# Optimization experiments

Measured on AMD Instinct MI355X. Metric: run time of the kernel, lower is better.

The kernel has to match this reference:

```python
import jax, jax.numpy as jnp
import numpy as np

WH, WW = 7, 7
N_TOK = WH * WW


def _buffers():
    # relative_coords_table: [1, 2*WH-1, 2*WW-1, 2], Swin-V2 log-spaced coords
    ch = np.arange(-(WH - 1), WH, dtype=np.float32)
    cw = np.arange(-(WW - 1), WW, dtype=np.float32)
    t = np.stack(np.meshgrid(ch, cw, indexing='ij'), axis=-1)[None]
    t[..., 0] /= (WH - 1)
    t[..., 1] /= (WW - 1)
    t *= 8.0
    t = np.sign(t) * np.log2(np.abs(t) + 1.0) / np.log2(8.0)
    # relative_position_index: [N, N]
    coords = np.stack(np.meshgrid(np.arange(WH), np.arange(WW), indexing='ij'))
    cf = coords.reshape(2, -1)
    rc = (cf[:, :, None] - cf[:, None, :]).transpose(1, 2, 0).astype(np.int32)
    rc[..., 0] += WH - 1
    rc[..., 1] += WW - 1
    rc[..., 0] *= 2 * WW - 1
    idx = rc.sum(-1)
    return jnp.asarray(t, jnp.float32), jnp.asarray(idx, jnp.int32)


def setup_inputs() -> dict:
    key = jax.random.key(0)
    ks = jax.random.split(key, 10)
    C, H = 384, 12
    B_, nW = 2048, 64
    rel_table, rel_index = _buffers()
    s = 0.02
    return {
        'x': jax.random.normal(ks[0], (B_, N_TOK, C), jnp.float32),
        'mask': jax.random.normal(ks[1], (nW, N_TOK, N_TOK), jnp.float32),
        'qkv_w': jax.random.normal(ks[2], (3 * C, C), jnp.float32) * s,
        'q_bias': jnp.zeros((C,), jnp.float32),
        'v_bias': jnp.zeros((C,), jnp.float32),
        'logit_scale': jnp.full((H, 1, 1), np.log(10.0), jnp.float32),
        'cpb_w1': jax.random.normal(ks[3], (512, 2), jnp.float32) * s,
        'cpb_b1': jnp.zeros((512,), jnp.float32),
        'cpb_w2': jax.random.normal(ks[4], (H, 512), jnp.float32) * s,
        'proj_w': jax.random.normal(ks[5], (C, C), jnp.float32) * s,
        'proj_b': jnp.zeros((C,), jnp.float32),
        'rel_table': rel_table,
        'rel_index': rel_index,
    }


def reference(x, mask, qkv_w, q_bias, v_bias, logit_scale, cpb_w1, cpb_b1,
              cpb_w2, proj_w, proj_b, rel_table, rel_index):
    B_, N, C = x.shape
    H = logit_scale.shape[0]
    Dh = C // H
    nW = mask.shape[0]
    # qkv projection with q/v bias, zero bias for k
    qkv_bias = jnp.concatenate([q_bias, jnp.zeros_like(v_bias), v_bias])
    qkv = x @ qkv_w.T + qkv_bias                       # [B, N, 3C]
    qkv = qkv.reshape(B_, N, 3, H, Dh).transpose(2, 0, 3, 1, 4)
    q, k, v = qkv[0], qkv[1], qkv[2]                    # [B, H, N, Dh]
    # per-head clamped logit scale
    ls = jnp.exp(jnp.minimum(logit_scale, np.log(1.0 / 0.01)))  # [H,1,1]
    # continuous relative position bias via small MLP
    tbl = jax.nn.relu(rel_table @ cpb_w1.T + cpb_b1) @ cpb_w2.T  # [1,13,13,H]
    tbl = tbl.reshape(-1, H)
    rpb = tbl[rel_index.reshape(-1)].reshape(N, N, H).transpose(2, 0, 1)
    rpb = 16.0 * jax.nn.sigmoid(rpb)                    # [H, N, N]
    # cosine attention (kernel uses norm + 1e-6 in denominator)
    qn = q / (jnp.sqrt(jnp.sum(q * q, -1, keepdims=True)) + 1e-6)
    kn = k / (jnp.sqrt(jnp.sum(k * k, -1, keepdims=True)) + 1e-6)
    attn = jnp.einsum('bhnd,bhmd->bhnm', qn, kn) * ls[None]
    attn = attn + rpb[None]
    # shift mask: window index w = batch_index % nW
    attn = attn.reshape(B_ // nW, nW, H, N, N) + mask[None, :, None]
    attn = attn.reshape(B_, H, N, N)
    # stable softmax with kernel's +1e-6 in denominator
    m = jnp.max(attn, -1, keepdims=True)
    e = jnp.exp(attn - m)
    p = e / (jnp.sum(e, -1, keepdims=True) + 1e-6)
    out = jnp.einsum('bhnm,bhmd->bhnd', p, v)           # [B, H, N, Dh]
    out = out.transpose(0, 2, 1, 3).reshape(B_, N, C)
    return out @ proj_w.T + proj_b
```

## Files before the change

### kernel.cpp

```cpp
#include <hip/hip_runtime.h>
#include <hip/hip_bf16.h>

typedef __attribute__((ext_vector_type(8))) short bf16x8;
typedef __attribute__((ext_vector_type(4))) float f32x4;
typedef __attribute__((ext_vector_type(16))) float f32x16;
typedef __attribute__((ext_vector_type(8))) unsigned short u16x8;
typedef unsigned short ushort_t;

#define DEVFN static __device__ __forceinline__

DEVFN ushort_t f2bf(float f) {
  unsigned int u = __builtin_bit_cast(unsigned int, f);
  u += 0x7FFFu + ((u >> 16) & 1u);
  return (ushort_t)(u >> 16);
}

DEVFN unsigned int cvtpk_bf16(float lo, float hi) {
  unsigned int r;
  asm("v_cvt_pk_bf16_f32 %0, %1, %2" : "=v"(r) : "v"(lo), "v"(hi));
  return r;
}

DEVFN void gload_lds16(const ushort_t* g, ushort_t* l) {
  __builtin_amdgcn_global_load_lds(
      (const __attribute__((address_space(1))) void*)g,
      (__attribute__((address_space(3))) void*)l, 16, 0, 0);
}

DEVFN int xcd_swz(int bid, int nwg) {
  int q = nwg >> 3, r = nwg & 7;
  int xcd = bid & 7, u = bid >> 3;
  return (xcd < r ? xcd * (q + 1) : r * (q + 1) + (xcd - r) * q) + u;
}

__global__ void k_prep_w(const float* __restrict__ qkv_w, const float* __restrict__ proj_w,
                         const float* __restrict__ q_bias, const float* __restrict__ v_bias,
                         ushort_t* __restrict__ qkv_wb, ushort_t* __restrict__ proj_wb,
                         float* __restrict__ qkv_bias) {
  int gid = blockIdx.x * blockDim.x + threadIdx.x;
  int stride = gridDim.x * blockDim.x;
  for (int i = gid; i < 1152 * 384; i += stride) qkv_wb[i] = f2bf(qkv_w[i]);
  for (int i = gid; i < 384 * 384; i += stride) proj_wb[i] = f2bf(proj_w[i]);
  for (int i = gid; i < 1152; i += stride)
    qkv_bias[i] = (i < 384) ? q_bias[i] : ((i < 768) ? 0.f : v_bias[i - 768]);
}

__global__ void k_xb(const float* __restrict__ x, ushort_t* __restrict__ xb, long n4) {
  long gid = (long)blockIdx.x * blockDim.x + threadIdx.x;
  long stride = (long)gridDim.x * blockDim.x;
  for (long i = gid; i < n4; i += stride) {
    float4 v = reinterpret_cast<const float4*>(x)[i];
    unsigned long long pk = (unsigned long long)f2bf(v.x) |
                            ((unsigned long long)f2bf(v.y) << 16) |
                            ((unsigned long long)f2bf(v.z) << 32) |
                            ((unsigned long long)f2bf(v.w) << 48);
    reinterpret_cast<unsigned long long*>(xb)[i] = pk;
  }
}

__global__ void k_prep_cpb(const float* __restrict__ rel_table, const float* __restrict__ cpb_w1,
                           const float* __restrict__ cpb_b1, const float* __restrict__ cpb_w2,
                           const float* __restrict__ logit_scale,
                           float* __restrict__ tbl, float* __restrict__ ls) {
  int lane = threadIdx.x;
  if (blockIdx.x == 169) {
    if (lane < 12) ls[lane] = __expf(fminf(logit_scale[lane], 4.605170185988092f));
    return;
  }
  int row = blockIdx.x;
  float t0 = rel_table[row * 2 + 0], t1 = rel_table[row * 2 + 1];
  float acc[12];
#pragma unroll
  for (int h = 0; h < 12; h++) acc[h] = 0.f;
  for (int j = lane; j < 512; j += 64) {
    float hj = fmaxf(cpb_w1[j * 2] * t0 + cpb_w1[j * 2 + 1] * t1 + cpb_b1[j], 0.f);
#pragma unroll
    for (int h = 0; h < 12; h++) acc[h] += cpb_w2[h * 512 + j] * hj;
  }
#pragma unroll
  for (int h = 0; h < 12; h++) {
    float v = acc[h];
    v += __shfl_xor(v, 1);  v += __shfl_xor(v, 2);  v += __shfl_xor(v, 4);
    v += __shfl_xor(v, 8);  v += __shfl_xor(v, 16); v += __shfl_xor(v, 32);
    if (lane == 0) tbl[row * 12 + h] = v;
  }
}

__global__ void k_prep_comb(const float* __restrict__ tbl, const int* __restrict__ rel_index,
                            const float* __restrict__ mask, float* __restrict__ comb) {
  int gid = blockIdx.x * blockDim.x + threadIdx.x;
  if (gid >= 64 * 12 * 2401) return;
  int ij = gid % 2401;
  int h = (gid / 2401) % 12;
  int w = gid / (2401 * 12);
  float t = tbl[rel_index[ij] * 12 + h];
  comb[gid] = 16.f / (1.f + __expf(-t)) + mask[w * 2401 + ij];
}

__global__ void __launch_bounds__(512) k_qkv(const ushort_t* __restrict__ xb,
                                             const ushort_t* __restrict__ wb,
                                             const float* __restrict__ bias,
                                             const float* __restrict__ lsb,
                                             ushort_t* __restrict__ qkvn, int nmb) {
  __shared__ __align__(16) ushort_t As[128][64];
  __shared__ __align__(16) ushort_t Bs[128][64];
  const int tid = threadIdx.x;
  const int lane = tid & 63, wid = tid >> 6;
  const int wm = wid >> 2, wn = wid & 3;
  const int l15 = lane & 15, g = lane >> 4;
  const int t = xcd_swz(blockIdx.x, nmb * 9);
  const int m0 = (t / 9) * 128, n0 = (t % 9) * 128;
  f32x4 acc[4][2] = {};

  for (int kk = 0; kk < 6; kk++) {
    const int k0 = kk * 64;
    const ushort_t* ga = xb + (size_t)m0 * 384 + k0;
    const ushort_t* gb = wb + (size_t)n0 * 384 + k0;
    __syncthreads();
#pragma unroll
    for (int it = 0; it < 2; it++) {
      int i = wid * 64 + lane + it * 512;
      int r = i >> 3;
      int cg = (i & 7) ^ (r & 7);
      ushort_t* ldst = (ushort_t*)As + wid * 512 + it * 4096;
      gload_lds16(ga + (size_t)r * 384 + cg * 8, ldst);
      gload_lds16(gb + (size_t)r * 384 + cg * 8, (ushort_t*)Bs + wid * 512 + it * 4096);
    }
    __syncthreads();
#pragma unroll
    for (int ks = 0; ks < 64; ks += 32) {
      bf16x8 a[4], b[2];
#pragma unroll
      for (int mi = 0; mi < 4; mi++) {
        int row = wm * 64 + mi * 16 + l15;
        a[mi] = *reinterpret_cast<const bf16x8*>(&As[row][((((ks >> 3) + g) ^ (row & 7))) * 8]);
      }
#pragma unroll
      for (int ni = 0; ni < 2; ni++) {
        int row = wn * 32 + ni * 16 + l15;
        b[ni] = *reinterpret_cast<const bf16x8*>(&Bs[row][((((ks >> 3) + g) ^ (row & 7))) * 8]);
      }
#pragma unroll
      for (int mi = 0; mi < 4; mi++)
#pragma unroll
        for (int ni = 0; ni < 2; ni++)
          acc[mi][ni] = __builtin_amdgcn_mfma_f32_16x16x32_bf16(a[mi], b[ni], acc[mi][ni], 0, 0, 0);
    }
  }
  const int colbase = n0 + wn * 32;
  const int which = colbase / 384;
  const float scl = (which == 0) ? lsb[colbase >> 5] : 1.f;
  const float b0 = bias[colbase + l15];
  const float b1 = bias[colbase + 16 + l15];
#pragma unroll
  for (int mi = 0; mi < 4; mi++) {
#pragma unroll
    for (int r = 0; r < 4; r++) {
      float v0 = acc[mi][0][r] + b0;
      float v1 = acc[mi][1][r] + b1;
      if (which < 2) {
        float ss = v0 * v0 + v1 * v1;
        ss += __shfl_xor(ss, 1);
        ss += __shfl_xor(ss, 2);
        ss += __shfl_xor(ss, 4);
        ss += __shfl_xor(ss, 8);
        float rn = scl / (sqrtf(ss) + 1e-6f);
        v0 *= rn; v1 *= rn;
      }
      int row = m0 + wm * 64 + mi * 16 + g * 4 + r;
      size_t base = (size_t)row * 1152 + colbase + l15;
      qkvn[base] = f2bf(v0);
      qkvn[base + 16] = f2bf(v1);
    }
  }
}

__global__ void __launch_bounds__(256, 4) k_attn(const ushort_t* __restrict__ qkvn,
                                                 const float* __restrict__ comb,
                                                 ushort_t* __restrict__ attn,
                                                 int win_base, int nk) {
  __shared__ float comb_s[2401];
  __shared__ __align__(16) ushort_t Vt[4][32][72];
  const int tid = threadIdx.x;
  const int lane = tid & 63, wv = tid >> 6;
  const int l31 = lane & 31, hi = lane >> 5;
  const int h = blockIdx.y;
  const int wloc = blockIdx.x & 63;
  const int k = (blockIdx.x >> 6) * 4 + wv;
  const bool active = k < nk;
  const int w_abs = (win_base + wloc) & 63;

  {
    const float* ct = comb + ((size_t)w_abs * 12 + h) * 2401;
    for (int i = tid; i < 2401; i += 256) comb_s[i] = ct[i];
  }

  const size_t rowbase = (size_t)(wloc + 64 * k) * 49;

  if (active) {
#pragma unroll
    for (int pass = 0; pass < 4; pass++) {
      int t = pass * 16 + (lane >> 2);
      int d0 = (lane & 3) * 8;
      u16x8 v = {};
      if (t < 49)
        v = *reinterpret_cast<const u16x8*>(&qkvn[(rowbase + t) * 1152 + 768 + h * 32 + d0]);
#pragma unroll
      for (int j = 0; j < 8; j++) Vt[wv][d0 + j][t] = v[j];
    }
  }
  __syncthreads();
  if (!active) return;

  bf16x8 qf[2][2], kf[2][2];
#pragma unroll
  for (int b = 0; b < 2; b++) {
    int t = b * 32 + l31; if (t > 48) t = 48;
    size_t rb = (rowbase + t) * 1152 + h * 32 + hi * 8;
#pragma unroll
    for (int ks = 0; ks < 2; ks++) {
      qf[b][ks] = *reinterpret_cast<const bf16x8*>(&qkvn[rb + ks * 16]);
      kf[b][ks] = *reinterpret_cast<const bf16x8*>(&qkvn[rb + 384 + ks * 16]);
    }
  }
  f32x16 S[2][2] = {};
#pragma unroll
  for (int a = 0; a < 2; a++)
#pragma unroll
    for (int b = 0; b < 2; b++) {
      S[a][b] = __builtin_amdgcn_mfma_f32_32x32x16_bf16(kf[a][0], qf[b][0], S[a][b], 0, 0, 0);
      S[a][b] = __builtin_amdgcn_mfma_f32_32x32x16_bf16(kf[a][1], qf[b][1], S[a][b], 0, 0, 0);
    }

#pragma unroll
  for (int b = 0; b < 2; b++) {
    const int qt = b * 32 + l31;
    const int qi = qt > 48 ? 48 : qt;
    const float* crow_p = &comb_s[qi * 49];
    float m = -3.0e38f;
#pragma unroll
    for (int a = 0; a < 2; a++)
#pragma unroll
      for (int r = 0; r < 16; r++) {
        int kt = a * 32 + (r & 3) + 8 * (r >> 2) + 4 * hi;
        float v = (kt < 49) ? (S[a][b][r] + crow_p[kt]) : -3.0e38f;
        S[a][b][r] = v;
        m = fmaxf(m, v);
      }
    m = fmaxf(m, __shfl_xor(m, 32));
    float s = 0.f;
#pragma unroll
    for (int a = 0; a < 2; a++)
#pragma unroll
      for (int r = 0; r < 16; r++) {
        float e = __expf(S[a][b][r] - m);
        S[a][b][r] = e;
        s += e;
      }
    s += __shfl_xor(s, 32);
    const float inv = 1.f / (s + 1e-6f);
    unsigned int pkk[2][4][2];
#pragma unroll
    for (int a = 0; a < 2; a++)
#pragma unroll
      for (int c = 0; c < 4; c++) {
        pkk[a][c][0] = cvtpk_bf16(S[a][b][c * 4 + 0] * inv, S[a][b][c * 4 + 1] * inv);
        pkk[a][c][1] = cvtpk_bf16(S[a][b][c * 4 + 2] * inv, S[a][b][c * 4 + 3] * inv);
      }
    f32x16 O = {};
#pragma unroll
    for (int a = 0; a < 2; a++)
#pragma unroll
      for (int ks = 0; ks < 2; ks++) {
        unsigned int s0 = hi ? pkk[a][2 * ks][0] : pkk[a][2 * ks + 1][0];
        unsigned int s1 = hi ? pkk[a][2 * ks][1] : pkk[a][2 * ks + 1][1];
        unsigned int r0 = __shfl_xor(s0, 32);
        unsigned int r1 = __shfl_xor(s1, 32);
        unsigned int w0 = hi ? r0 : pkk[a][2 * ks][0];
        unsigned int w1 = hi ? r1 : pkk[a][2 * ks][1];
        unsigned int w2 = hi ? pkk[a][2 * ks + 1][0] : r0;
        unsigned int w3 = hi ? pkk[a][2 * ks + 1][1] : r1;
        uint4 wq = {w0, w1, w2, w3};
        bf16x8 pa = __builtin_bit_cast(bf16x8, wq);
        bf16x8 vb = *reinterpret_cast<const bf16x8*>(&Vt[wv][l31][a * 32 + ks * 16 + hi * 8]);
        O = __builtin_amdgcn_mfma_f32_32x32x16_bf16(pa, vb, O, 0, 0, 0);
      }
#pragma unroll
    for (int r = 0; r < 16; r++) {
      int qrow = b * 32 + (r & 3) + 8 * (r >> 2) + 4 * hi;
      if (qrow < 49)
        attn[(rowbase + qrow) * 384 + h * 32 + l31] = f2bf(O[r]);
    }
  }
}

__global__ void __launch_bounds__(512) k_proj(const ushort_t* __restrict__ a,
                                              const ushort_t* __restrict__ wb,
                                              const float* __restrict__ pbias,
                                              float* __restrict__ out, int nmb) {
  __shared__ __align__(16) ushort_t As[128][64];
  __shared__ __align__(16) ushort_t Bs[128][64];
  const int tid = threadIdx.x;
  const int lane = tid & 63, wid = tid >> 6;
  const int wm = wid >> 2, wn = wid & 3;
  const int l15 = lane & 15, g = lane >> 4;
  const int t = xcd_swz(blockIdx.x, nmb * 3);
  const int m0 = (t / 3) * 128, n0 = (t % 3) * 128;
  f32x4 acc[4][2] = {};

  for (int kk = 0; kk < 6; kk++) {
    const int k0 = kk * 64;
    const ushort_t* ga = a + (size_t)m0 * 384 + k0;
    const ushort_t* gb = wb + (size_t)n0 * 384 + k0;
    __syncthreads();
#pragma unroll
    for (int it = 0; it < 2; it++) {
      int i = wid * 64 + lane + it * 512;
      int r = i >> 3;
      int cg = (i & 7) ^ (r & 7);
      gload_lds16(ga + (size_t)r * 384 + cg * 8, (ushort_t*)As + wid * 512 + it * 4096);
      gload_lds16(gb + (size_t)r * 384 + cg * 8, (ushort_t*)Bs + wid * 512 + it * 4096);
    }
    __syncthreads();
#pragma unroll
    for (int ks = 0; ks < 64; ks += 32) {
      bf16x8 av[4], bv[2];
#pragma unroll
      for (int mi = 0; mi < 4; mi++) {
        int row = wm * 64 + mi * 16 + l15;
        av[mi] = *reinterpret_cast<const bf16x8*>(&As[row][((((ks >> 3) + g) ^ (row & 7))) * 8]);
      }
#pragma unroll
      for (int ni = 0; ni < 2; ni++) {
        int row = wn * 32 + ni * 16 + l15;
        bv[ni] = *reinterpret_cast<const bf16x8*>(&Bs[row][((((ks >> 3) + g) ^ (row & 7))) * 8]);
      }
#pragma unroll
      for (int mi = 0; mi < 4; mi++)
#pragma unroll
        for (int ni = 0; ni < 2; ni++)
          acc[mi][ni] = __builtin_amdgcn_mfma_f32_16x16x32_bf16(av[mi], bv[ni], acc[mi][ni], 0, 0, 0);
    }
  }
  const int colbase = n0 + wn * 32;
  const float b0 = pbias[colbase + l15];
  const float b1 = pbias[colbase + 16 + l15];
#pragma unroll
  for (int mi = 0; mi < 4; mi++)
#pragma unroll
    for (int r = 0; r < 4; r++) {
      int row = m0 + wm * 64 + mi * 16 + g * 4 + r;
      out[(size_t)row * 384 + colbase + l15] = acc[mi][0][r] + b0;
      out[(size_t)row * 384 + colbase + 16 + l15] = acc[mi][1][r] + b1;
    }
}

extern "C" void kernel_launch(void* const* d_in, const int* in_sizes, int n_in,
                              void* d_out, int out_size, void* d_ws, size_t ws_size,
                              hipStream_t stream) {
  const float* x        = (const float*)d_in[0];
  const float* mask     = (const float*)d_in[1];
  const float* qkv_w    = (const float*)d_in[2];
  const float* q_bias   = (const float*)d_in[3];
  const float* v_bias   = (const float*)d_in[4];
  const float* logit_sc = (const float*)d_in[5];
  const float* cpb_w1   = (const float*)d_in[6];
  const float* cpb_b1   = (const float*)d_in[7];
  const float* cpb_w2   = (const float*)d_in[8];
  const float* proj_w   = (const float*)d_in[9];
  const float* proj_b   = (const float*)d_in[10];
  const float* rel_tab  = (const float*)d_in[11];
  const int*   rel_idx  = (const int*)d_in[12];
  float* out = (float*)d_out;

  char* p = (char*)d_ws;
  auto carve = [&](size_t bytes) { char* r = p; p += (bytes + 255) & ~(size_t)255; return r; };
  ushort_t* qkv_wb  = (ushort_t*)carve(1152 * 384 * 2);
  ushort_t* proj_wb = (ushort_t*)carve(384 * 384 * 2);
  float* qkv_bias   = (float*)carve(1152 * 4);
  float* tbl        = (float*)carve(169 * 12 * 4);
  float* lsb        = (float*)carve(12 * 4);
  float* comb       = (float*)carve((size_t)64 * 12 * 2401 * 4);
  size_t fixed = (size_t)(p - (char*)d_ws);
  size_t avail = ws_size > fixed ? ws_size - fixed : 0;

  int nc = 1;
  while (nc < 16) {
    size_t per = ((size_t)(2048 / nc)) * 49 * (384 + 1152 + 384) * 2 + (1 << 20);
    if (per <= avail) break;
    nc *= 2;
  }
  const int nwin = 2048 / nc;
  const size_t Mc = (size_t)nwin * 49;
  ushort_t* xbuf  = (ushort_t*)carve(Mc * 384 * 2);
  ushort_t* qkvn  = (ushort_t*)carve(Mc * 1152 * 2);
  ushort_t* attnb = (ushort_t*)carve(Mc * 384 * 2);
  const int nmb = (int)(Mc / 128);
  const int nk = nwin >> 6;

  k_prep_w<<<dim3(512), dim3(256), 0, stream>>>(qkv_w, proj_w, q_bias, v_bias, qkv_wb, proj_wb, qkv_bias);
  k_prep_cpb<<<dim3(170), dim3(64), 0, stream>>>(rel_tab, cpb_w1, cpb_b1, cpb_w2, logit_sc, tbl, lsb);
  k_prep_comb<<<dim3((64 * 12 * 2401 + 255) / 256), dim3(256), 0, stream>>>(tbl, rel_idx, mask, comb);

  for (int c = 0; c < nc; c++) {
    size_t roff = (size_t)c * Mc;
    k_xb<<<dim3(2048), dim3(256), 0, stream>>>(x + roff * 384, xbuf, (long)(Mc * 384 / 4));
    k_qkv<<<dim3(nmb * 9), dim3(512), 0, stream>>>(xbuf, qkv_wb, qkv_bias, lsb, qkvn, nmb);
    k_attn<<<dim3(64 * ((nk + 3) / 4), 12), dim3(256), 0, stream>>>(qkvn, comb, attnb, c * nwin, nk);
    k_proj<<<dim3(nmb * 3), dim3(512), 0, stream>>>(attnb, proj_wb, proj_b, out + roff * 384, nmb);
  }
}
```

Before: 413.5 us.

## Double-buffer LDS tiles in QKV and projection GEMMs to overlap loads

Both GEMM kernels now keep two LDS buffers per operand and issue the global-to-LDS loads for the next K-slice before running the MFMA work on the current slice, with one barrier per iteration. The aim is to hide global load latency behind matrix math rather than stalling on two barriers per step. LDS use doubles to 64KB per block, which may lower occupancy. Correctness depends on the single barrier also waiting for the async global_load_lds writes, which the code does not wait on explicitly.

```diff
diff --git a/kernel.cpp b/kernel.cpp
--- a/kernel.cpp
+++ b/kernel.cpp
@@ -102,8 +102,8 @@
                                              const float* __restrict__ bias,
                                              const float* __restrict__ lsb,
                                              ushort_t* __restrict__ qkvn, int nmb) {
-  __shared__ __align__(16) ushort_t As[128][64];
-  __shared__ __align__(16) ushort_t Bs[128][64];
+  __shared__ __align__(16) ushort_t As[2][128][64];
+  __shared__ __align__(16) ushort_t Bs[2][128][64];
   const int tid = threadIdx.x;
   const int lane = tid & 63, wid = tid >> 6;
   const int wm = wid >> 2, wn = wid & 3;
@@ -112,33 +112,42 @@
   const int m0 = (t / 9) * 128, n0 = (t % 9) * 128;
   f32x4 acc[4][2] = {};
 
+  const int i0 = wid * 64 + lane;
+  const int r0_ = i0 >> 3, cg0 = (i0 & 7) ^ (r0_ & 7);
+  const int i1 = i0 + 512;
+  const int r1_ = i1 >> 3, cg1 = (i1 & 7) ^ (r1_ & 7);
+  const size_t ao0 = (size_t)r0_ * 384 + cg0 * 8;
+  const size_t ao1 = (size_t)r1_ * 384 + cg1 * 8;
+  const int ldsoff0 = wid * 512, ldsoff1 = wid * 512 + 4096;
+
+#define QKV_STAGE(s, kk)                                                    \
+  {                                                                         \
+    const ushort_t* ga = xb + (size_t)m0 * 384 + (kk) * 64;                 \
+    const ushort_t* gb = wb + (size_t)n0 * 384 + (kk) * 64;                 \
+    gload_lds16(ga + ao0, &As[s][0][0] + ldsoff0);                          \
+    gload_lds16(gb + ao0, &Bs[s][0][0] + ldsoff0);                          \
+    gload_lds16(ga + ao1, &As[s][0][0] + ldsoff1);                          \
+    gload_lds16(gb + ao1, &Bs[s][0][0] + ldsoff1);                          \
+  }
+
+  QKV_STAGE(0, 0);
+  __syncthreads();
+  int cur = 0;
+#pragma unroll
   for (int kk = 0; kk < 6; kk++) {
-    const int k0 = kk * 64;
-    const ushort_t* ga = xb + (size_t)m0 * 384 + k0;
-    const ushort_t* gb = wb + (size_t)n0 * 384 + k0;
-    __syncthreads();
-#pragma unroll
-    for (int it = 0; it < 2; it++) {
-      int i = wid * 64 + lane + it * 512;
-      int r = i >> 3;
-      int cg = (i & 7) ^ (r & 7);
-      ushort_t* ldst = (ushort_t*)As + wid * 512 + it * 4096;
-      gload_lds16(ga + (size_t)r * 384 + cg * 8, ldst);
-      gload_lds16(gb + (size_t)r * 384 + cg * 8, (ushort_t*)Bs + wid * 512 + it * 4096);
-    }
-    __syncthreads();
+    if (kk < 5) QKV_STAGE(cur ^ 1, kk + 1);
 #pragma unroll
     for (int ks = 0; ks < 64; ks += 32) {
       bf16x8 a[4], b[2];
 #pragma unroll
       for (int mi = 0; mi < 4; mi++) {
         int row = wm * 64 + mi * 16 + l15;
-        a[mi] = *reinterpret_cast<const bf16x8*>(&As[row][((((ks >> 3) + g) ^ (row & 7))) * 8]);
+        a[mi] = *reinterpret_cast<const bf16x8*>(&As[cur][row][((((ks >> 3) + g) ^ (row & 7))) * 8]);
       }
 #pragma unroll
       for (int ni = 0; ni < 2; ni++) {
         int row = wn * 32 + ni * 16 + l15;
-        b[ni] = *reinterpret_cast<const bf16x8*>(&Bs[row][((((ks >> 3) + g) ^ (row & 7))) * 8]);
+        b[ni] = *reinterpret_cast<const bf16x8*>(&Bs[cur][row][((((ks >> 3) + g) ^ (row & 7))) * 8]);
       }
 #pragma unroll
       for (int mi = 0; mi < 4; mi++)
@@ -146,7 +155,10 @@
         for (int ni = 0; ni < 2; ni++)
           acc[mi][ni] = __builtin_amdgcn_mfma_f32_16x16x32_bf16(a[mi], b[ni], acc[mi][ni], 0, 0, 0);
     }
-  }
+    __syncthreads();
+    cur ^= 1;
+  }
+#undef QKV_STAGE
   const int colbase = n0 + wn * 32;
   const int which = colbase / 384;
   const float scl = (which == 0) ? lsb[colbase >> 5] : 1.f;
@@ -298,8 +310,8 @@
                                               const ushort_t* __restrict__ wb,
                                               const float* __restrict__ pbias,
                                               float* __restrict__ out, int nmb) {
-  __shared__ __align__(16) ushort_t As[128][64];
-  __shared__ __align__(16) ushort_t Bs[128][64];
+  __shared__ __align__(16) ushort_t As[2][128][64];
+  __shared__ __align__(16) ushort_t Bs[2][128][64];
   const int tid = threadIdx.x;
   const int lane = tid & 63, wid = tid >> 6;
   const int wm = wid >> 2, wn = wid & 3;
@@ -308,32 +320,42 @@
   const int m0 = (t / 3) * 128, n0 = (t % 3) * 128;
   f32x4 acc[4][2] = {};
 
+  const int i0 = wid * 64 + lane;
+  const int r0_ = i0 >> 3, cg0 = (i0 & 7) ^ (r0_ & 7);
+  const int i1 = i0 + 512;
+  const int r1_ = i1 >> 3, cg1 = (i1 & 7) ^ (r1_ & 7);
+  const size_t ao0 = (size_t)r0_ * 384 + cg0 * 8;
+  const size_t ao1 = (size_t)r1_ * 384 + cg1 * 8;
+  const int ldsoff0 = wid * 512, ldsoff1 = wid * 512 + 4096;
+
+#define PRJ_STAGE(s, kk)                                                    \
+  {                                                                         \
+    const ushort_t* ga = a + (size_t)m0 * 384 + (kk) * 64;                  \
+    const ushort_t* gb = wb + (size_t)n0 * 384 + (kk) * 64;                 \
+    gload_lds16(ga + ao0, &As[s][0][0] + ldsoff0);                          \
+    gload_lds16(gb + ao0, &Bs[s][0][0] + ldsoff0);                          \
+    gload_lds16(ga + ao1, &As[s][0][0] + ldsoff1);                          \
+    gload_lds16(gb + ao1, &Bs[s][0][0] + ldsoff1);                          \
+  }
+
+  PRJ_STAGE(0, 0);
+  __syncthreads();
+  int cur = 0;
+#pragma unroll
   for (int kk = 0; kk < 6; kk++) {
-    const int k0 = kk * 64;
-    const ushort_t* ga = a + (size_t)m0 * 384 + k0;
-    const ushort_t* gb = wb + (size_t)n0 * 384 + k0;
-    __syncthreads();
-#pragma unroll
-    for (int it = 0; it < 2; it++) {
-      int i = wid * 64 + lane + it * 512;
-      int r = i >> 3;
-      int cg = (i & 7) ^ (r & 7);
-      gload_lds16(ga + (size_t)r * 384 + cg * 8, (ushort_t*)As + wid * 512 + it * 4096);
-      gload_lds16(gb + (size_t)r * 384 + cg * 8, (ushort_t*)Bs + wid * 512 + it * 4096);
-    }
-    __syncthreads();
+    if (kk < 5) PRJ_STAGE(cur ^ 1, kk + 1);
 #pragma unroll
     for (int ks = 0; ks < 64; ks += 32) {
       bf16x8 av[4], bv[2];
 #pragma unroll
       for (int mi = 0; mi < 4; mi++) {
         int row = wm * 64 + mi * 16 + l15;
-        av[mi] = *reinterpret_cast<const bf16x8*>(&As[row][((((ks >> 3) + g) ^ (row & 7))) * 8]);
+        av[mi] = *reinterpret_cast<const bf16x8*>(&As[cur][row][((((ks >> 3) + g) ^ (row & 7))) * 8]);
       }
 #pragma unroll
       for (int ni = 0; ni < 2; ni++) {
         int row = wn * 32 + ni * 16 + l15;
-        bv[ni] = *reinterpret_cast<const bf16x8*>(&Bs[row][((((ks >> 3) + g) ^ (row & 7))) * 8]);
+        bv[ni] = *reinterpret_cast<const bf16x8*>(&Bs[cur][row][((((ks >> 3) + g) ^ (row & 7))) * 8]);
       }
 #pragma unroll
       for (int mi = 0; mi < 4; mi++)
@@ -341,7 +363,10 @@
         for (int ni = 0; ni < 2; ni++)
           acc[mi][ni] = __builtin_amdgcn_mfma_f32_16x16x32_bf16(av[mi], bv[ni], acc[mi][ni], 0, 0, 0);
     }
-  }
+    __syncthreads();
+    cur ^= 1;
+  }
+#undef PRJ_STAGE
   const int colbase = n0 + wn * 32;
   const float b0 = pbias[colbase + l15];
   const float b1 = pbias[colbase + 16 + l15];
```

Result: slower. 434.6 us (+5.1%).
